# Kernel tuning notes

Measured on AMD Instinct MI355X. Metric: run time of the kernel, lower is better.

The kernel has to match this reference:

```python
import jax, jax.numpy as jnp
import numpy as np
from math import pi as PI, log

B, N, D, K = 16, 16384, 64, 64


def setup_inputs() -> dict:
    key = jax.random.key(0)
    k1, k2, k3, k4 = jax.random.split(key, 4)
    x = jax.random.normal(k1, (B, N, D), dtype=jnp.float32)
    pi_w = jax.nn.softmax(jax.random.normal(k2, (K,), dtype=jnp.float32))  # mixture weights, sum to 1
    mu = jax.random.normal(k3, (K, D), dtype=jnp.float32)
    var = jax.random.uniform(k4, (K, D), dtype=jnp.float32, minval=0.5, maxval=1.5)  # diagonal variances
    return {"x": x, "pi": pi_w, "mu": mu, "var": var}


def reference(x, pi, mu, var):
    b, n, d = x.shape
    # --- gmm.predict_proba: diagonal-covariance Gaussian log-likelihoods + log pi, softmax over K ---
    inv_var = 1.0 / var                                   # (K, D)
    x2 = x * x                                            # (B, N, D)
    # Mahalanobis distance expanded via matmuls to avoid a (B,N,K,D) intermediate
    maha = (jnp.einsum('bnd,kd->bnk', x2, inv_var)
            - 2.0 * jnp.einsum('bnd,kd->bnk', x, mu * inv_var)
            + jnp.sum(mu * mu * inv_var, axis=-1))        # (B, N, K)
    log_det = jnp.sum(jnp.log(var), axis=-1)              # (K,)
    log_prob = -0.5 * (d * log(2.0 * PI) + log_det + maha)
    Q = jax.nn.softmax(log_prob + jnp.log(pi), axis=-1)   # (B, N, K) responsibilities
    # --- weighted reductions over N ---
    Q_sum = jnp.sum(Q, axis=1) / n                         # (B, K)
    Q_x = jnp.einsum('bnk,bnd->bkd', Q, x) / n             # (B, K, D)
    Q_x2 = jnp.einsum('bnk,bnd->bkd', Q, x2) / n           # (B, K, D)
    # --- Fisher-vector statistics ---
    d_pi = Q_sum - pi                                      # (B, K)
    qs = Q_sum[..., None]                                  # (B, K, 1)
    d_mu = Q_x - qs * mu
    d_sigma = -Q_x2 - qs * (mu * mu) + qs * var + 2.0 * Q_x * mu
    return jnp.concatenate([d_pi.reshape(b, -1), d_mu.reshape(b, -1), d_sigma.reshape(b, -1)], axis=1)
```

## Files before the change

### kernel.cpp

```cpp
#include <hip/hip_runtime.h>
#include <hip/hip_bf16.h>
#include <math.h>

#define B_  16
#define N_  16384
#define D_  64
#define K_  64
#define OUT_PER_B (K_ + 2*K_*D_)
#define PART_FLOATS OUT_PER_B
#define CHUNKS 32
#define NTILES (N_ / CHUNKS / 64)

#define WS_C0_OFF   4096
#define WS_PART_OFF 4160

typedef float f32x4 __attribute__((ext_vector_type(4)));
typedef short short8 __attribute__((ext_vector_type(8)));

union U8 { short8 s8; unsigned int u[4]; };

__device__ __forceinline__ unsigned short f2bf(float f) {
    union { float f; unsigned int u; } v; v.f = f;
    unsigned int r = v.u + 0x7FFFu + ((v.u >> 16) & 1u);
    return (unsigned short)(r >> 16);
}

__device__ __forceinline__ unsigned int f2bf2(float lo, float hi) {
    __hip_bfloat162 h = __float22bfloat162_rn(make_float2(lo, hi));
    unsigned int u;
    __builtin_memcpy(&u, &h, 4);
    return u;
}

__global__ __launch_bounds__(256) void fv_prep(const float* __restrict__ pi,
                                               const float* __restrict__ mu,
                                               const float* __restrict__ var,
                                               float* __restrict__ ws) {
    __shared__ float red[256];
    int t = threadIdx.x;
    unsigned short* wt = (unsigned short*)ws;
    for (int i = t; i < 4096; i += 256) {
        int k = i >> 6, d = i & 63;
        float v  = var[i];
        float m  = mu[i];
        float iv = 1.0f / v;
        wt[k * 128 + d]      = f2bf(-0.5f * iv);
        wt[k * 128 + 64 + d] = f2bf(m * iv);
    }
    int k = t >> 2, pr = t & 3;
    float s = 0.0f;
    #pragma unroll
    for (int j = 0; j < 16; ++j) {
        int d = pr * 16 + j;
        float v = var[k * 64 + d];
        float m = mu[k * 64 + d];
        s += __logf(v) + m * m / v;
    }
    red[t] = s;
    __syncthreads();
    if (pr == 0) {
        float sum = red[4 * k] + red[4 * k + 1] + red[4 * k + 2] + red[4 * k + 3];
        ws[WS_C0_OFF + k] = __logf(pi[k]) - 0.5f * (117.6241322502f + sum);
    }
}

__global__ __launch_bounds__(256, 2) void fv_main(const float* __restrict__ x,
                                                  const float* __restrict__ ws,
                                                  float* __restrict__ partials) {
    __shared__ __align__(16) unsigned short QtS[2][64 * 72];
    __shared__ float qsum_s[4][64];

    const int t    = threadIdx.x;
    const int w    = t >> 6;
    const int lane = t & 63;
    const int r16  = lane & 15;
    const int q    = lane >> 4;

    short8 wfrag[4][4];
    f32x4  c0v[4];
    {
        const unsigned short* wsu = (const unsigned short*)ws;
        #pragma unroll
        for (int kt = 0; kt < 4; ++kt) {
            const unsigned short* wr = wsu + (16 * kt + r16) * 128 + 8 * q;
            #pragma unroll
            for (int h = 0; h < 4; ++h)
                wfrag[kt][h] = *(const short8*)(const void*)(wr + 32 * h);
            c0v[kt] = *(const f32x4*)(ws + WS_C0_OFF + 16 * kt + 4 * q);
        }
    }

    const int bi    = blockIdx.y;
    const int chunk = blockIdx.x;
    const int ppb   = N_ / CHUNKS;
    const float* xb = x + ((size_t)bi * N_ + (size_t)chunk * ppb) * D_;

    f32x4 accX[4]  = {};
    f32x4 accX2[4] = {};
    float qsacc[4][4] = {};

    const int rowoff = (16 * w + r16) * D_ + 8 * q;
    const int dcol   = 16 * w + r16;

    float4 va, vb, vc, vd;
    float  vle[16];
    {
        const float* xr = xb + rowoff;
        va = *(const float4*)(xr);
        vb = *(const float4*)(xr + 4);
        vc = *(const float4*)(xr + 32);
        vd = *(const float4*)(xr + 36);
        const float* xc = xb + dcol;
        #pragma unroll
        for (int c = 0; c < 2; ++c)
            #pragma unroll
            for (int j = 0; j < 8; ++j)
                vle[8 * c + j] = xc[(32 * c + 8 * q + j) * D_];
    }

    #pragma unroll 2
    for (int tile = 0; tile < NTILES; ++tile) {
        float4 nva, nvb, nvc, nvd;
        float  nvle[16];
        if (tile + 1 < NTILES) {
            const float* xtn = xb + (size_t)(tile + 1) * 64 * D_;
            const float* xr = xtn + rowoff;
            nva = *(const float4*)(xr);
            nvb = *(const float4*)(xr + 4);
            nvc = *(const float4*)(xr + 32);
            nvd = *(const float4*)(xr + 36);
            const float* xc = xtn + dcol;
            #pragma unroll
            for (int c = 0; c < 2; ++c)
                #pragma unroll
                for (int j = 0; j < 8; ++j)
                    nvle[8 * c + j] = xc[(32 * c + 8 * q + j) * D_];
        }

        U8 fxa, fxb, fx2a, fx2b;
        fxa.u[0]  = f2bf2(va.x, va.y);           fxa.u[1]  = f2bf2(va.z, va.w);
        fxa.u[2]  = f2bf2(vb.x, vb.y);           fxa.u[3]  = f2bf2(vb.z, vb.w);
        fxb.u[0]  = f2bf2(vc.x, vc.y);           fxb.u[1]  = f2bf2(vc.z, vc.w);
        fxb.u[2]  = f2bf2(vd.x, vd.y);           fxb.u[3]  = f2bf2(vd.z, vd.w);
        fx2a.u[0] = f2bf2(va.x*va.x, va.y*va.y); fx2a.u[1] = f2bf2(va.z*va.z, va.w*va.w);
        fx2a.u[2] = f2bf2(vb.x*vb.x, vb.y*vb.y); fx2a.u[3] = f2bf2(vb.z*vb.z, vb.w*vb.w);
        fx2b.u[0] = f2bf2(vc.x*vc.x, vc.y*vc.y); fx2b.u[1] = f2bf2(vc.z*vc.z, vc.w*vc.w);
        fx2b.u[2] = f2bf2(vd.x*vd.x, vd.y*vd.y); fx2b.u[3] = f2bf2(vd.z*vd.z, vd.w*vd.w);

        float sc[4][4];
        #pragma unroll
        for (int kt = 0; kt < 4; ++kt) {
            f32x4 a = c0v[kt];
            a = __builtin_amdgcn_mfma_f32_16x16x32_bf16(wfrag[kt][0], fx2a.s8, a, 0, 0, 0);
            a = __builtin_amdgcn_mfma_f32_16x16x32_bf16(wfrag[kt][1], fx2b.s8, a, 0, 0, 0);
            a = __builtin_amdgcn_mfma_f32_16x16x32_bf16(wfrag[kt][2], fxa.s8,  a, 0, 0, 0);
            a = __builtin_amdgcn_mfma_f32_16x16x32_bf16(wfrag[kt][3], fxb.s8,  a, 0, 0, 0);
            sc[kt][0] = a[0]; sc[kt][1] = a[1]; sc[kt][2] = a[2]; sc[kt][3] = a[3];
        }

        float mx = sc[0][0];
        #pragma unroll
        for (int kt = 0; kt < 4; ++kt)
            #pragma unroll
            for (int rr = 0; rr < 4; ++rr) mx = fmaxf(mx, sc[kt][rr]);
        mx = fmaxf(mx, __shfl_xor(mx, 16));
        mx = fmaxf(mx, __shfl_xor(mx, 32));
        float z = 0.0f;
        #pragma unroll
        for (int kt = 0; kt < 4; ++kt)
            #pragma unroll
            for (int rr = 0; rr < 4; ++rr) {
                sc[kt][rr] = __expf(sc[kt][rr] - mx);
                z += sc[kt][rr];
            }
        z += __shfl_xor(z, 16);
        z += __shfl_xor(z, 32);
        float inv = 1.0f / z;
        const int p = 16 * w + r16;
        unsigned short* Qb = QtS[tile & 1];
        #pragma unroll
        for (int kt = 0; kt < 4; ++kt) {
            #pragma unroll
            for (int rr = 0; rr < 4; ++rr) {
                float qv = sc[kt][rr] * inv;
                qsacc[kt][rr] += qv;
                Qb[(16 * kt + 4 * q + rr) * 72 + p] = f2bf(qv);
            }
        }

        __syncthreads();

        U8 fxp0, fxp1, fx2p0, fx2p1;
        #pragma unroll
        for (int i = 0; i < 4; ++i) {
            float a0 = vle[2 * i], a1 = vle[2 * i + 1];
            float b0 = vle[8 + 2 * i], b1 = vle[8 + 2 * i + 1];
            fxp0.u[i]  = f2bf2(a0, a1);
            fxp1.u[i]  = f2bf2(b0, b1);
            fx2p0.u[i] = f2bf2(a0 * a0, a1 * a1);
            fx2p1.u[i] = f2bf2(b0 * b0, b1 * b1);
        }
        #pragma unroll
        for (int kt = 0; kt < 4; ++kt) {
            const unsigned short* qr = &Qb[(16 * kt + r16) * 72 + 8 * q];
            short8 aq0 = *(const short8*)(const void*)(qr);
            short8 aq1 = *(const short8*)(const void*)(qr + 32);
            accX[kt]  = __builtin_amdgcn_mfma_f32_16x16x32_bf16(aq0, fxp0.s8,  accX[kt],  0, 0, 0);
            accX2[kt] = __builtin_amdgcn_mfma_f32_16x16x32_bf16(aq0, fx2p0.s8, accX2[kt], 0, 0, 0);
            accX[kt]  = __builtin_amdgcn_mfma_f32_16x16x32_bf16(aq1, fxp1.s8,  accX[kt],  0, 0, 0);
            accX2[kt] = __builtin_amdgcn_mfma_f32_16x16x32_bf16(aq1, fx2p1.s8, accX2[kt], 0, 0, 0);
        }

        va = nva; vb = nvb; vc = nvc; vd = nvd;
        #pragma unroll
        for (int i = 0; i < 16; ++i) vle[i] = nvle[i];
    }

    float* part = partials + ((size_t)bi * CHUNKS + chunk) * PART_FLOATS;
    #pragma unroll
    for (int kt = 0; kt < 4; ++kt)
        #pragma unroll
        for (int rr = 0; rr < 4; ++rr) {
            int k = 16 * kt + 4 * q + rr;
            part[64 + k * 64 + 16 * w + r16]        = accX[kt][rr];
            part[64 + 4096 + k * 64 + 16 * w + r16] = accX2[kt][rr];
        }
    #pragma unroll
    for (int kt = 0; kt < 4; ++kt)
        #pragma unroll
        for (int rr = 0; rr < 4; ++rr) {
            float v = qsacc[kt][rr];
            v += __shfl_xor(v, 1);
            v += __shfl_xor(v, 2);
            v += __shfl_xor(v, 4);
            v += __shfl_xor(v, 8);
            if (r16 == 0) qsum_s[w][16 * kt + 4 * q + rr] = v;
        }
    __syncthreads();
    if (t < 64)
        part[t] = qsum_s[0][t] + qsum_s[1][t] + qsum_s[2][t] + qsum_s[3][t];
}

__global__ __launch_bounds__(256) void fv_finalize(const float* __restrict__ pi,
                                                   const float* __restrict__ mu,
                                                   const float* __restrict__ var,
                                                   const float* __restrict__ partials,
                                                   float* __restrict__ out,
                                                   int chunks) {
    int g = blockIdx.x * 256 + threadIdx.x;
    if (g >= B_ * OUT_PER_B) return;
    int b   = g / OUT_PER_B;
    int pos = g - b * OUT_PER_B;
    const float* base = partials + (size_t)b * chunks * PART_FLOATS;
    const float invN = 1.0f / (float)N_;

    if (pos < 64) {
        float qs = 0.0f;
        for (int c = 0; c < chunks; ++c) qs += base[c * PART_FLOATS + pos];
        out[g] = qs * invN - pi[pos];
    } else if (pos < 64 + 4096) {
        int idx = pos - 64;
        int k = idx >> 6;
        float qs = 0.0f, qx = 0.0f;
        for (int c = 0; c < chunks; ++c) {
            qs += base[c * PART_FLOATS + k];
            qx += base[c * PART_FLOATS + pos];
        }
        out[g] = (qx - qs * mu[idx]) * invN;
    } else {
        int idx = pos - 64 - 4096;
        int k = idx >> 6;
        float qs = 0.0f, qx = 0.0f, qx2 = 0.0f;
        for (int c = 0; c < chunks; ++c) {
            qs  += base[c * PART_FLOATS + k];
            qx  += base[c * PART_FLOATS + 64 + idx];
            qx2 += base[c * PART_FLOATS + pos];
        }
        float m = mu[idx], v = var[idx];
        out[g] = (-qx2 - qs * m * m + qs * v + 2.0f * qx * m) * invN;
    }
}

extern "C" void kernel_launch(void* const* d_in, const int* in_sizes, int n_in,
                              void* d_out, int out_size, void* d_ws, size_t ws_size,
                              hipStream_t stream) {
    const float* x   = (const float*)d_in[0];
    const float* pi  = (const float*)d_in[1];
    const float* mu  = (const float*)d_in[2];
    const float* var = (const float*)d_in[3];
    float* ws = (float*)d_ws;
    float* partials = ws + WS_PART_OFF;

    fv_prep<<<1, 256, 0, stream>>>(pi, mu, var, ws);
    fv_main<<<dim3(CHUNKS, B_), 256, 0, stream>>>(x, ws, partials);
    int total = B_ * OUT_PER_B;
    fv_finalize<<<(total + 255) / 256, 256, 0, stream>>>(pi, mu, var, partials,
                                                         (float*)d_out, CHUNKS);
}
```

Before: 128.3 us.

## Store partials as bf16, load column x in-tile, use raw barrier, pack Q stores

Per-chunk partial accumulators for Q·x and Q·x² are now written as bf16 rather than fp32, halving partial-buffer traffic for both the main and finalize kernels. The strided column loads of x are no longer software-prefetched a tile ahead; they are issued in the current tile just before the barrier, which lowers register pressure. The __syncthreads is replaced by an inline s_waitcnt lgkmcnt(0) plus s_barrier, and Q values are converted to bf16 in pairs. Rounding partial sums to bf16 before the cross-chunk reduction adds precision loss, and the column loads are now exposed latency instead of overlapping the previous tile.

```diff
diff --git a/kernel.cpp b/kernel.cpp
--- a/kernel.cpp
+++ b/kernel.cpp
@@ -7,12 +7,12 @@
 #define D_  64
 #define K_  64
 #define OUT_PER_B (K_ + 2*K_*D_)
-#define PART_FLOATS OUT_PER_B
 #define CHUNKS 32
 #define NTILES (N_ / CHUNKS / 64)
 
 #define WS_C0_OFF   4096
 #define WS_PART_OFF 4160
+#define PART_STRIDE (64*4 + 2*4096*2)
 
 typedef float f32x4 __attribute__((ext_vector_type(4)));
 typedef short short8 __attribute__((ext_vector_type(8)));
@@ -30,6 +30,13 @@
     unsigned int u;
     __builtin_memcpy(&u, &h, 4);
     return u;
+}
+
+__device__ __forceinline__ float bf2f(unsigned short u) {
+    unsigned int v = ((unsigned int)u) << 16;
+    float f;
+    __builtin_memcpy(&f, &v, 4);
+    return f;
 }
 
 __global__ __launch_bounds__(256) void fv_prep(const float* __restrict__ pi,
@@ -66,7 +73,7 @@
 
 __global__ __launch_bounds__(256, 2) void fv_main(const float* __restrict__ x,
                                                   const float* __restrict__ ws,
-                                                  float* __restrict__ partials) {
+                                                  char* __restrict__ partials) {
     __shared__ __align__(16) unsigned short QtS[2][64 * 72];
     __shared__ float qsum_s[4][64];
 
@@ -103,38 +110,25 @@
     const int dcol   = 16 * w + r16;
 
     float4 va, vb, vc, vd;
-    float  vle[16];
     {
         const float* xr = xb + rowoff;
         va = *(const float4*)(xr);
         vb = *(const float4*)(xr + 4);
         vc = *(const float4*)(xr + 32);
         vd = *(const float4*)(xr + 36);
-        const float* xc = xb + dcol;
-        #pragma unroll
-        for (int c = 0; c < 2; ++c)
-            #pragma unroll
-            for (int j = 0; j < 8; ++j)
-                vle[8 * c + j] = xc[(32 * c + 8 * q + j) * D_];
     }
 
     #pragma unroll 2
     for (int tile = 0; tile < NTILES; ++tile) {
+        const float* xt = xb + (size_t)tile * 64 * D_;
+
         float4 nva, nvb, nvc, nvd;
-        float  nvle[16];
         if (tile + 1 < NTILES) {
-            const float* xtn = xb + (size_t)(tile + 1) * 64 * D_;
-            const float* xr = xtn + rowoff;
+            const float* xr = xt + 64 * D_ + rowoff;
             nva = *(const float4*)(xr);
             nvb = *(const float4*)(xr + 4);
             nvc = *(const float4*)(xr + 32);
             nvd = *(const float4*)(xr + 36);
-            const float* xc = xtn + dcol;
-            #pragma unroll
-            for (int c = 0; c < 2; ++c)
-                #pragma unroll
-                for (int j = 0; j < 8; ++j)
-                    nvle[8 * c + j] = xc[(32 * c + 8 * q + j) * D_];
         }
 
         U8 fxa, fxb, fx2a, fx2b;
@@ -181,14 +175,28 @@
         #pragma unroll
         for (int kt = 0; kt < 4; ++kt) {
             #pragma unroll
-            for (int rr = 0; rr < 4; ++rr) {
-                float qv = sc[kt][rr] * inv;
-                qsacc[kt][rr] += qv;
-                Qb[(16 * kt + 4 * q + rr) * 72 + p] = f2bf(qv);
+            for (int rr = 0; rr < 4; rr += 2) {
+                float q0 = sc[kt][rr] * inv;
+                float q1 = sc[kt][rr + 1] * inv;
+                qsacc[kt][rr]     += q0;
+                qsacc[kt][rr + 1] += q1;
+                unsigned int pk = f2bf2(q0, q1);
+                Qb[(16 * kt + 4 * q + rr)     * 72 + p] = (unsigned short)pk;
+                Qb[(16 * kt + 4 * q + rr + 1) * 72 + p] = (unsigned short)(pk >> 16);
             }
         }
 
-        __syncthreads();
+        float vle[16];
+        {
+            const float* xc = xt + dcol;
+            #pragma unroll
+            for (int c = 0; c < 2; ++c)
+                #pragma unroll
+                for (int j = 0; j < 8; ++j)
+                    vle[8 * c + j] = xc[(32 * c + 8 * q + j) * D_];
+        }
+
+        asm volatile("s_waitcnt lgkmcnt(0)\n\ts_barrier" ::: "memory");
 
         U8 fxp0, fxp1, fx2p0, fx2p1;
         #pragma unroll
@@ -212,18 +220,19 @@
         }
 
         va = nva; vb = nvb; vc = nvc; vd = nvd;
-        #pragma unroll
-        for (int i = 0; i < 16; ++i) vle[i] = nvle[i];
-    }
-
-    float* part = partials + ((size_t)bi * CHUNKS + chunk) * PART_FLOATS;
+    }
+
+    char* rec = partials + ((size_t)bi * CHUNKS + chunk) * PART_STRIDE;
+    float* part_qs = (float*)rec;
+    unsigned short* part_qx  = (unsigned short*)(rec + 256);
+    unsigned short* part_qx2 = part_qx + 4096;
     #pragma unroll
     for (int kt = 0; kt < 4; ++kt)
         #pragma unroll
         for (int rr = 0; rr < 4; ++rr) {
             int k = 16 * kt + 4 * q + rr;
-            part[64 + k * 64 + 16 * w + r16]        = accX[kt][rr];
-            part[64 + 4096 + k * 64 + 16 * w + r16] = accX2[kt][rr];
+            part_qx [k * 64 + 16 * w + r16] = f2bf(accX[kt][rr]);
+            part_qx2[k * 64 + 16 * w + r16] = f2bf(accX2[kt][rr]);
         }
     #pragma unroll
     for (int kt = 0; kt < 4; ++kt)
@@ -238,43 +247,45 @@
         }
     __syncthreads();
     if (t < 64)
-        part[t] = qsum_s[0][t] + qsum_s[1][t] + qsum_s[2][t] + qsum_s[3][t];
+        part_qs[t] = qsum_s[0][t] + qsum_s[1][t] + qsum_s[2][t] + qsum_s[3][t];
 }
 
 __global__ __launch_bounds__(256) void fv_finalize(const float* __restrict__ pi,
                                                    const float* __restrict__ mu,
                                                    const float* __restrict__ var,
-                                                   const float* __restrict__ partials,
-                                                   float* __restrict__ out,
-                                                   int chunks) {
+                                                   const char* __restrict__ partials,
+                                                   float* __restrict__ out) {
     int g = blockIdx.x * 256 + threadIdx.x;
     if (g >= B_ * OUT_PER_B) return;
     int b   = g / OUT_PER_B;
     int pos = g - b * OUT_PER_B;
-    const float* base = partials + (size_t)b * chunks * PART_FLOATS;
+    const char* base = partials + (size_t)b * CHUNKS * PART_STRIDE;
     const float invN = 1.0f / (float)N_;
 
     if (pos < 64) {
         float qs = 0.0f;
-        for (int c = 0; c < chunks; ++c) qs += base[c * PART_FLOATS + pos];
+        for (int c = 0; c < CHUNKS; ++c)
+            qs += ((const float*)(base + c * PART_STRIDE))[pos];
         out[g] = qs * invN - pi[pos];
     } else if (pos < 64 + 4096) {
         int idx = pos - 64;
         int k = idx >> 6;
         float qs = 0.0f, qx = 0.0f;
-        for (int c = 0; c < chunks; ++c) {
-            qs += base[c * PART_FLOATS + k];
-            qx += base[c * PART_FLOATS + pos];
+        for (int c = 0; c < CHUNKS; ++c) {
+            const char* r = base + c * PART_STRIDE;
+            qs += ((const float*)r)[k];
+            qx += bf2f(((const unsigned short*)(r + 256))[idx]);
         }
         out[g] = (qx - qs * mu[idx]) * invN;
     } else {
         int idx = pos - 64 - 4096;
         int k = idx >> 6;
         float qs = 0.0f, qx = 0.0f, qx2 = 0.0f;
-        for (int c = 0; c < chunks; ++c) {
-            qs  += base[c * PART_FLOATS + k];
-            qx  += base[c * PART_FLOATS + 64 + idx];
-            qx2 += base[c * PART_FLOATS + pos];
+        for (int c = 0; c < CHUNKS; ++c) {
+            const char* r = base + c * PART_STRIDE;
+            qs  += ((const float*)r)[k];
+            qx  += bf2f(((const unsigned short*)(r + 256))[idx]);
+            qx2 += bf2f(((const unsigned short*)(r + 256))[4096 + idx]);
         }
         float m = mu[idx], v = var[idx];
         out[g] = (-qx2 - qs * m * m + qs * v + 2.0f * qx * m) * invN;
@@ -289,11 +300,11 @@
     const float* mu  = (const float*)d_in[2];
     const float* var = (const float*)d_in[3];
     float* ws = (float*)d_ws;
-    float* partials = ws + WS_PART_OFF;
+    char* partials = (char*)(ws + WS_PART_OFF);
 
     fv_prep<<<1, 256, 0, stream>>>(pi, mu, var, ws);
     fv_main<<<dim3(CHUNKS, B_), 256, 0, stream>>>(x, ws, partials);
     int total = B_ * OUT_PER_B;
     fv_finalize<<<(total + 255) / 256, 256, 0, stream>>>(pi, mu, var, partials,
-                                                         (float*)d_out, CHUNKS);
-}
+                                                         (float*)d_out);
+}
```

New measurement: 120.6 us. -6.0%, faster.
